# Kernel tuning notes

Measured on AMD Instinct MI355X. Metric: run time of the kernel, lower is better.

## Reference

```python
import jax, jax.numpy as jnp
import numpy as np

N_NODES = 50000
N_EDGES = 300000
D = 256
EPS = 1e-12


def setup_inputs() -> dict:
    key = jax.random.key(0)
    ks = jax.random.split(key, 10)
    h5_all = jax.random.normal(ks[0], (N_NODES, D), dtype=jnp.float32)
    edge_index = jax.random.randint(ks[1], (2, N_EDGES), 0, N_NODES, dtype=jnp.int64)
    edge_weight = jax.random.uniform(ks[2], (N_EDGES,), dtype=jnp.float32)
    s = 1.0 / np.sqrt(D)
    W6 = jax.random.normal(ks[3], (D, D), dtype=jnp.float32) * s
    b6 = jnp.zeros((D,), dtype=jnp.float32)
    W7 = jax.random.normal(ks[4], (D, D), dtype=jnp.float32) * s
    b7 = jnp.zeros((D,), dtype=jnp.float32)
    Wp = jax.random.normal(ks[5], (D, D), dtype=jnp.float32) * s
    bp = jnp.zeros((D,), dtype=jnp.float32)
    return {"h5_all": h5_all, "edge_index": edge_index, "edge_weight": edge_weight,
            "W6": W6, "b6": b6, "W7": W7, "b7": b7, "Wp": Wp, "bp": bp}


def _gcn_layer(x, W, b, src, dst, norm, n_nodes):
    # x: [N, D]; transform then gather-scale-scatter along edges
    xt = x @ W                                   # [N, D]
    msg = xt[src] * norm[:, None]                # [E, D] gathered + scaled
    agg = jax.ops.segment_sum(msg, dst, num_segments=n_nodes)  # [N, D]
    return jax.nn.relu(agg + b)


def reference(h5_all, edge_index, edge_weight, W6, b6, W7, b7, Wp, bp):
    src, dst = edge_index[0], edge_index[1]
    # symmetric degree normalization with edge weights (GCN-style)
    deg_out = jax.ops.segment_sum(edge_weight, src, num_segments=N_NODES)
    deg_in = jax.ops.segment_sum(edge_weight, dst, num_segments=N_NODES)
    norm = edge_weight * jax.lax.rsqrt(deg_out[src] * deg_in[dst] + EPS)  # [E]
    h6 = _gcn_layer(h5_all, W6, b6, src, dst, norm, N_NODES)
    h7 = _gcn_layer(h6, W7, b7, src, dst, norm, N_NODES)
    out = h7 @ Wp + bp                           # post_mp linear head
    return out
```

## Files before the change

kernel.cpp:

```cpp
#include <hip/hip_runtime.h>

#define N_NODES 50000
#define N_PANELS 3125
#define N_EDGES 300000
#define EPS_F 1e-12f
#define DEGB 64
#define WB 96
#define AB (N_NODES * 32 / 256)
#define FILLB 128
#define GB 512
#define SCAN_NB ((N_NODES + 255) / 256)
#define ZBYTES (N_NODES * 8)

typedef _Float16 f16x8 __attribute__((ext_vector_type(8)));
typedef float f32x4 __attribute__((ext_vector_type(4)));

static __device__ inline f32x4 mfma_f16(f16x8 a, f16x8 b, f32x4 c) {
    return __builtin_amdgcn_mfma_f32_16x16x32_f16(a, b, c, 0, 0, 0);
}

static __device__ inline size_t swz(int row, int l) {
    return ((size_t)(row >> 4) * 8 + (l >> 2)) * 512 + (size_t)((l & 3) * 128 + (row & 15) * 8);
}


__global__ __launch_bounds__(256) void zero_kernel(int4* __restrict__ p, int n16) {
    int i = blockIdx.x * 256 + threadIdx.x;
    if (i < n16) p[i] = make_int4(0, 0, 0, 0);
}


__global__ __launch_bounds__(256) void p1_kernel(const int* __restrict__ ei,
                                                 const float* __restrict__ ew,
                                                 unsigned* __restrict__ pk_out,
                                                 unsigned* __restrict__ pk_in,
                                                 unsigned* __restrict__ rank,
                                                 const float* __restrict__ W6,
                                                 const float* __restrict__ W7,
                                                 const float* __restrict__ Wp,
                                                 _Float16* __restrict__ Bsw,
                                                 const float* __restrict__ h5,
                                                 _Float16* __restrict__ Asw) {
    int b = blockIdx.x;
    if (b < DEGB) {
        for (int e = b * 256 + (int)threadIdx.x; e < N_EDGES; e += DEGB * 256) {
            int s = ei[e];
            int d = ei[N_EDGES + e];
            unsigned wfx = (unsigned)(ew[e] * 262144.0f);
            atomicAdd(&pk_out[s], wfx);
            unsigned old = atomicAdd(&pk_in[d], (1u << 24) | wfx);
            rank[e] = old >> 24;
        }
    } else if (b < DEGB + WB) {
        int bb = b - DEGB;
        int wsel = bb >> 5;
        const float* W = (wsel == 0) ? W6 : (wsel == 1) ? W7 : Wp;
        int id = (bb & 31) * 256 + threadIdx.x;
        int n = id >> 5, l = id & 31;
        f16x8 o;
#pragma unroll
        for (int j = 0; j < 8; ++j)
            o[j] = (_Float16)W[(l * 8 + j) * 256 + n];
        *(f16x8*)&Bsw[(size_t)wsel * 65536 + swz(n, l)] = o;
    } else {
        int tid = (b - DEGB - WB) * 256 + threadIdx.x;
        int row = tid >> 5, l = tid & 31;
        const float* p = &h5[(size_t)row * 256 + l * 8];
        float4 v0 = *(const float4*)p;
        float4 v1 = *(const float4*)(p + 4);
        f16x8 o;
        o[0] = (_Float16)v0.x; o[1] = (_Float16)v0.y;
        o[2] = (_Float16)v0.z; o[3] = (_Float16)v0.w;
        o[4] = (_Float16)v1.x; o[5] = (_Float16)v1.y;
        o[6] = (_Float16)v1.z; o[7] = (_Float16)v1.w;
        *(f16x8*)&Asw[swz(row, l)] = o;
    }
}


__global__ __launch_bounds__(256) void scan1_kernel(const unsigned* __restrict__ pk_in,
                                                    const unsigned* __restrict__ pk_out,
                                                    float* __restrict__ deg_in,
                                                    float* __restrict__ deg_out,
                                                    int* __restrict__ partial) {
    __shared__ int sh[256];
    int i = blockIdx.x * 256 + threadIdx.x;
    int c = 0;
    if (i < N_NODES) {
        unsigned p = pk_in[i];
        c = (int)(p >> 24);
        deg_in[i] = (float)(p & 0xFFFFFFu) * 0x1p-18f;
        deg_out[i] = (float)pk_out[i] * 0x1p-18f;
    }
    sh[threadIdx.x] = c;
    __syncthreads();
    for (int off = 128; off > 0; off >>= 1) {
        if (threadIdx.x < (unsigned)off) sh[threadIdx.x] += sh[threadIdx.x + off];
        __syncthreads();
    }
    if (threadIdx.x == 0) partial[blockIdx.x] = sh[0];
}

__global__ __launch_bounds__(256) void scan23_kernel(const unsigned* __restrict__ pk_in,
                                                     const int* __restrict__ partial,
                                                     int* __restrict__ row_ptr) {
    __shared__ int ps[256];
    __shared__ int sh[256];
    int t = threadIdx.x;
    int pv = (t < SCAN_NB) ? partial[t] : 0;
    ps[t] = pv;
    __syncthreads();
    for (int off = 1; off < 256; off <<= 1) {
        int x = (t >= off) ? ps[t - off] : 0;
        __syncthreads();
        ps[t] += x;
        __syncthreads();
    }
    int incl = ps[t];
    __syncthreads();
    ps[t] = incl - pv;
    __syncthreads();
    const int boff = ps[blockIdx.x];

    int i = blockIdx.x * 256 + t;
    int v = (i < N_NODES) ? (int)(pk_in[i] >> 24) : 0;
    sh[t] = v;
    __syncthreads();
    for (int off = 1; off < 256; off <<= 1) {
        int x = (t >= off) ? sh[t - off] : 0;
        __syncthreads();
        sh[t] += x;
        __syncthreads();
    }
    if (i < N_NODES) row_ptr[i] = sh[t] - v + boff;
    if (i == 0) row_ptr[N_NODES] = N_EDGES;
}


__global__ __launch_bounds__(256) void p2_kernel(const int* __restrict__ ei,
                                                 const float* __restrict__ ew,
                                                 const unsigned* __restrict__ rank,
                                                 const float* __restrict__ deg_out,
                                                 const float* __restrict__ deg_in,
                                                 const int* __restrict__ row_ptr,
                                                 int2* __restrict__ csr,
                                                 const _Float16* __restrict__ Asw,
                                                 const _Float16* __restrict__ Bsw,
                                                 _Float16* __restrict__ xt) {
    __shared__ __align__(16) _Float16 ebuf[4][16 * 72];

    if (blockIdx.x < FILLB) {
        for (int e = blockIdx.x * 256 + (int)threadIdx.x; e < N_EDGES; e += FILLB * 256) {
            int s = ei[e];
            int d = ei[N_EDGES + e];
            float nm = ew[e] * rsqrtf(deg_out[s] * deg_in[d] + EPS_F);
            csr[row_ptr[d] + (int)rank[e]] = make_int2(s, __float_as_int(nm));
        }
        return;
    }

    const int t = threadIdx.x;
    const int w = t >> 6, lane = t & 63;

    f16x8 bf[4][8];
#pragma unroll
    for (int cp4 = 0; cp4 < 4; ++cp4)
#pragma unroll
        for (int kb = 0; kb < 8; ++kb)
            bf[cp4][kb] = *(const f16x8*)&Bsw[(size_t)((w * 4 + cp4) * 8 + kb) * 512 + lane * 8];

    for (int p = blockIdx.x - FILLB; p < N_PANELS; p += GB) {
        const _Float16* abase = &Asw[(size_t)p * 4096 + lane * 8];
        f16x8 af[8];
#pragma unroll
        for (int kb = 0; kb < 8; ++kb)
            af[kb] = *(const f16x8*)&abase[kb * 512];

        f32x4 acc[4];
#pragma unroll
        for (int cp4 = 0; cp4 < 4; ++cp4) acc[cp4] = (f32x4){0.f, 0.f, 0.f, 0.f};
#pragma unroll
        for (int kb = 0; kb < 8; ++kb)
#pragma unroll
            for (int cp4 = 0; cp4 < 4; ++cp4)
                acc[cp4] = mfma_f16(af[kb], bf[cp4][kb], acc[cp4]);

        _Float16* eb = ebuf[w];
        const int rq = 4 * (lane >> 4);
        const int lr = lane & 15;
#pragma unroll
        for (int cp4 = 0; cp4 < 4; ++cp4)
#pragma unroll
            for (int rr = 0; rr < 4; ++rr)
                eb[(rq + rr) * 72 + cp4 * 16 + lr] = (_Float16)acc[cp4][rr];
#pragma unroll
        for (int it = 0; it < 2; ++it) {
            int rl = it * 8 + (lane >> 3);
            f16x8 v = *(const f16x8*)&eb[rl * 72 + (lane & 7) * 8];
            *(f16x8*)&xt[(size_t)(p * 16 + rl) * 256 + w * 64 + (lane & 7) * 8] = v;
        }
    }
}


template <int MODE>
__global__ __launch_bounds__(256) void gemm_f16(const _Float16* __restrict__ Asw,
                                                const _Float16* __restrict__ Bsw,
                                                const float* __restrict__ bias,
                                                void* __restrict__ Cout) {
    __shared__ __align__(16) char ebraw[4][16 * 68 * 4];

    const int t = threadIdx.x;
    const int w = t >> 6, lane = t & 63;
    const int lr = lane & 15;

    f16x8 bf[4][8];
#pragma unroll
    for (int cp4 = 0; cp4 < 4; ++cp4)
#pragma unroll
        for (int kb = 0; kb < 8; ++kb)
            bf[cp4][kb] = *(const f16x8*)&Bsw[(size_t)((w * 4 + cp4) * 8 + kb) * 512 + lane * 8];

    float bc[4];
    if (MODE == 1) {
#pragma unroll
        for (int cp4 = 0; cp4 < 4; ++cp4) bc[cp4] = bias[w * 64 + cp4 * 16 + lr];
    }

    for (int p = blockIdx.x; p < N_PANELS; p += GB) {
        const _Float16* abase = &Asw[(size_t)p * 4096 + lane * 8];
        f16x8 af[8];
#pragma unroll
        for (int kb = 0; kb < 8; ++kb)
            af[kb] = *(const f16x8*)&abase[kb * 512];

        f32x4 acc[4];
#pragma unroll
        for (int cp4 = 0; cp4 < 4; ++cp4) acc[cp4] = (f32x4){0.f, 0.f, 0.f, 0.f};
#pragma unroll
        for (int kb = 0; kb < 8; ++kb)
#pragma unroll
            for (int cp4 = 0; cp4 < 4; ++cp4)
                acc[cp4] = mfma_f16(af[kb], bf[cp4][kb], acc[cp4]);

        const int rq = 4 * (lane >> 4);
        if (MODE == 0) {
            _Float16* eb = (_Float16*)ebraw[w];
#pragma unroll
            for (int cp4 = 0; cp4 < 4; ++cp4)
#pragma unroll
                for (int rr = 0; rr < 4; ++rr)
                    eb[(rq + rr) * 72 + cp4 * 16 + lr] = (_Float16)acc[cp4][rr];
            _Float16* xp = (_Float16*)Cout;
#pragma unroll
            for (int it = 0; it < 2; ++it) {
                int rl = it * 8 + (lane >> 3);
                f16x8 v = *(const f16x8*)&eb[rl * 72 + (lane & 7) * 8];
                *(f16x8*)&xp[(size_t)(p * 16 + rl) * 256 + w * 64 + (lane & 7) * 8] = v;
            }
        } else {
            float* eb = (float*)ebraw[w];
#pragma unroll
            for (int cp4 = 0; cp4 < 4; ++cp4)
#pragma unroll
                for (int rr = 0; rr < 4; ++rr)
                    eb[(rq + rr) * 68 + cp4 * 16 + lr] = acc[cp4][rr] + bc[cp4];
            float* op = (float*)Cout;
#pragma unroll
            for (int it = 0; it < 4; ++it) {
                int rl = it * 4 + (lane >> 4);
                float4 v = *(const float4*)&eb[rl * 68 + lr * 4];
                *(float4*)&op[(size_t)(p * 16 + rl) * 256 + w * 64 + lr * 4] = v;
            }
        }
    }
}


__global__ __launch_bounds__(256) void agg_kernel(const _Float16* __restrict__ xt,
                                                  const int* __restrict__ row_ptr,
                                                  const int2* __restrict__ csr,
                                                  const float* __restrict__ bias,
                                                  _Float16* __restrict__ Asw) {
    const int g = threadIdx.x >> 5;
    const int l = threadIdx.x & 31;
    const int v = blockIdx.x * 8 + g;
    const int d0 = l * 8;

    const int s0 = row_ptr[v];
    const int s1 = row_ptr[v + 1];

    float acc[8] = {0.f, 0.f, 0.f, 0.f, 0.f, 0.f, 0.f, 0.f};

    int i = s0;
    for (; i + 4 <= s1; i += 4) {
        int2 hd[4];
#pragma unroll
        for (int u = 0; u < 4; ++u) hd[u] = csr[i + u];
        f16x8 val[4];
#pragma unroll
        for (int u = 0; u < 4; ++u)
            val[u] = *(const f16x8*)&xt[(size_t)hd[u].x * 256 + d0];
#pragma unroll
        for (int u = 0; u < 4; ++u) {
            float wv = __int_as_float(hd[u].y);
#pragma unroll
            for (int j = 0; j < 8; ++j)
                acc[j] += (float)val[u][j] * wv;
        }
    }
    {
        int rem = s1 - i;
        int2 hd[3];
#pragma unroll
        for (int u = 0; u < 3; ++u)
            hd[u] = (u < rem) ? csr[i + u] : make_int2(0, 0);
        f16x8 val[3];
#pragma unroll
        for (int u = 0; u < 3; ++u)
            val[u] = *(const f16x8*)&xt[(size_t)hd[u].x * 256 + d0];
#pragma unroll
        for (int u = 0; u < 3; ++u) {
            float wv = __int_as_float(hd[u].y);
#pragma unroll
            for (int j = 0; j < 8; ++j)
                acc[j] += (float)val[u][j] * wv;
        }
    }

    f16x8 o;
#pragma unroll
    for (int j = 0; j < 8; ++j) {
        float r = acc[j] + bias[d0 + j];
        r = r > 0.f ? r : 0.f;
        o[j] = (_Float16)r;
    }
    *(f16x8*)&Asw[swz(v, l)] = o;
}


extern "C" void kernel_launch(void* const* d_in, const int* in_sizes, int n_in,
                              void* d_out, int out_size, void* d_ws, size_t ws_size,
                              hipStream_t stream) {
    (void)in_sizes; (void)n_in; (void)out_size; (void)ws_size;
    const float* h5 = (const float*)d_in[0];
    const int*   ei = (const int*)d_in[1];
    const float* ew = (const float*)d_in[2];
    const float* W6 = (const float*)d_in[3];
    const float* b6 = (const float*)d_in[4];
    const float* W7 = (const float*)d_in[5];
    const float* b7 = (const float*)d_in[6];
    const float* Wp = (const float*)d_in[7];
    const float* bp = (const float*)d_in[8];
    float* out = (float*)d_out;

    char* ws = (char*)d_ws;
    size_t off = 0;
    auto alloc = [&](size_t bytes) -> void* {
        void* p = ws + off;
        off = (off + bytes + 255) & ~(size_t)255;
        return p;
    };

    char* zblk = (char*)alloc(ZBYTES);
    unsigned* pk_out = (unsigned*)zblk;
    unsigned* pk_in  = (unsigned*)(zblk + N_NODES * 4);

    unsigned* rank  = (unsigned*)alloc(N_EDGES * 4);
    float* deg_out = (float*)alloc(N_NODES * 4);
    float* deg_in  = (float*)alloc(N_NODES * 4);
    int*   row_ptr = (int*)alloc((N_NODES + 1) * 4);
    int*   partial = (int*)alloc(SCAN_NB * 4);
    int2*  csr     = (int2*)alloc(N_EDGES * 8);
    _Float16* Bsw  = (_Float16*)alloc(3 * 65536 * 2);
    _Float16* Asw  = (_Float16*)alloc((size_t)N_NODES * 256 * 2);
    _Float16* xt   = (_Float16*)alloc((size_t)N_NODES * 256 * 2);

    const int Z16 = ZBYTES / 16;

    zero_kernel<<<(Z16 + 255) / 256, 256, 0, stream>>>((int4*)zblk, Z16);

    p1_kernel<<<DEGB + WB + AB, 256, 0, stream>>>(ei, ew, pk_out, pk_in, rank,
                                                  W6, W7, Wp, Bsw, h5, Asw);

    scan1_kernel<<<SCAN_NB, 256, 0, stream>>>(pk_in, pk_out, deg_in, deg_out, partial);
    scan23_kernel<<<SCAN_NB, 256, 0, stream>>>(pk_in, partial, row_ptr);

    p2_kernel<<<FILLB + GB, 256, 0, stream>>>(ei, ew, rank, deg_out, deg_in, row_ptr,
                                              csr, Asw, Bsw, xt);

    agg_kernel<<<N_NODES / 8, 256, 0, stream>>>(xt, row_ptr, csr, b6, Asw);
    gemm_f16<0><<<GB, 256, 0, stream>>>(Asw, Bsw + 65536, nullptr, xt);
    agg_kernel<<<N_NODES / 8, 256, 0, stream>>>(xt, row_ptr, csr, b7, Asw);
    gemm_f16<1><<<GB, 256, 0, stream>>>(Asw, Bsw + 2 * 65536, bp, out);
}
```

Measured before the change: 160.5 us.

## Fuse h5 fp16 conversion into first GEMM and reschedule setup kernels

The first transform GEMM now reads h5 in fp32 directly, converts it to fp16 through a shared-memory tile, and multiplies, so the separate swizzled Asw staging pass, with its write and reread of a 25 MB fp16 copy, is gone. The zeroing and weight swizzle are merged into one init kernel. The degree atomics now run alongside the GEMM, and the CSR fill moves to its own kernel after the scan. This adds two block barriers per panel and makes the CSR fill a standalone launch that no longer overlaps the GEMM.

```diff
diff --git a/kernel.cpp b/kernel.cpp
--- a/kernel.cpp
+++ b/kernel.cpp
@@ -5,8 +5,8 @@
 #define N_EDGES 300000
 #define EPS_F 1e-12f
 #define DEGB 64
+#define ZB 98
 #define WB 96
-#define AB (N_NODES * 32 / 256)
 #define FILLB 128
 #define GB 512
 #define SCAN_NB ((N_NODES + 255) / 256)
@@ -24,23 +24,41 @@
 }
 
 
-__global__ __launch_bounds__(256) void zero_kernel(int4* __restrict__ p, int n16) {
-    int i = blockIdx.x * 256 + threadIdx.x;
-    if (i < n16) p[i] = make_int4(0, 0, 0, 0);
-}
-
-
-__global__ __launch_bounds__(256) void p1_kernel(const int* __restrict__ ei,
+__global__ __launch_bounds__(256) void init_kernel(int4* __restrict__ z,
+                                                   const float* __restrict__ W6,
+                                                   const float* __restrict__ W7,
+                                                   const float* __restrict__ Wp,
+                                                   _Float16* __restrict__ Bsw) {
+    int b = blockIdx.x;
+    if (b < ZB) {
+        int i = b * 256 + threadIdx.x;
+        if (i < ZBYTES / 16) z[i] = make_int4(0, 0, 0, 0);
+    } else {
+        int bb = b - ZB;
+        int wsel = bb >> 5;
+        const float* W = (wsel == 0) ? W6 : (wsel == 1) ? W7 : Wp;
+        int id = (bb & 31) * 256 + threadIdx.x;
+        int n = id >> 5, l = id & 31;
+        f16x8 o;
+#pragma unroll
+        for (int j = 0; j < 8; ++j)
+            o[j] = (_Float16)W[(l * 8 + j) * 256 + n];
+        *(f16x8*)&Bsw[(size_t)wsel * 65536 + swz(n, l)] = o;
+    }
+}
+
+
+__global__ __launch_bounds__(256) void pA_kernel(const int* __restrict__ ei,
                                                  const float* __restrict__ ew,
                                                  unsigned* __restrict__ pk_out,
                                                  unsigned* __restrict__ pk_in,
                                                  unsigned* __restrict__ rank,
-                                                 const float* __restrict__ W6,
-                                                 const float* __restrict__ W7,
-                                                 const float* __restrict__ Wp,
-                                                 _Float16* __restrict__ Bsw,
                                                  const float* __restrict__ h5,
-                                                 _Float16* __restrict__ Asw) {
+                                                 const _Float16* __restrict__ Bsw,
+                                                 _Float16* __restrict__ xt) {
+    __shared__ __align__(16) _Float16 atile[16 * 264];
+    __shared__ __align__(16) _Float16 ebuf[4][16 * 72];
+
     int b = blockIdx.x;
     if (b < DEGB) {
         for (int e = b * 256 + (int)threadIdx.x; e < N_EDGES; e += DEGB * 256) {
@@ -51,29 +69,67 @@
             unsigned old = atomicAdd(&pk_in[d], (1u << 24) | wfx);
             rank[e] = old >> 24;
         }
-    } else if (b < DEGB + WB) {
-        int bb = b - DEGB;
-        int wsel = bb >> 5;
-        const float* W = (wsel == 0) ? W6 : (wsel == 1) ? W7 : Wp;
-        int id = (bb & 31) * 256 + threadIdx.x;
-        int n = id >> 5, l = id & 31;
-        f16x8 o;
-#pragma unroll
-        for (int j = 0; j < 8; ++j)
-            o[j] = (_Float16)W[(l * 8 + j) * 256 + n];
-        *(f16x8*)&Bsw[(size_t)wsel * 65536 + swz(n, l)] = o;
-    } else {
-        int tid = (b - DEGB - WB) * 256 + threadIdx.x;
-        int row = tid >> 5, l = tid & 31;
-        const float* p = &h5[(size_t)row * 256 + l * 8];
-        float4 v0 = *(const float4*)p;
-        float4 v1 = *(const float4*)(p + 4);
-        f16x8 o;
-        o[0] = (_Float16)v0.x; o[1] = (_Float16)v0.y;
-        o[2] = (_Float16)v0.z; o[3] = (_Float16)v0.w;
-        o[4] = (_Float16)v1.x; o[5] = (_Float16)v1.y;
-        o[6] = (_Float16)v1.z; o[7] = (_Float16)v1.w;
-        *(f16x8*)&Asw[swz(row, l)] = o;
+        return;
+    }
+
+    const int t = threadIdx.x;
+    const int w = t >> 6, lane = t & 63;
+    const int srow = t >> 4;
+    const int scol = (t & 15) * 16;
+
+    f16x8 bf[4][8];
+#pragma unroll
+    for (int cp4 = 0; cp4 < 4; ++cp4)
+#pragma unroll
+        for (int kb = 0; kb < 8; ++kb)
+            bf[cp4][kb] = *(const f16x8*)&Bsw[(size_t)((w * 4 + cp4) * 8 + kb) * 512 + lane * 8];
+
+    for (int p = b - DEGB; p < N_PANELS; p += GB) {
+        const float* src = &h5[(size_t)(p * 16 + srow) * 256 + scol];
+        f16x8 c0, c1;
+#pragma unroll
+        for (int q = 0; q < 2; ++q) {
+            float4 v0 = *(const float4*)(src + q * 8);
+            float4 v1 = *(const float4*)(src + q * 8 + 4);
+            f16x8& cc = q ? c1 : c0;
+            cc[0] = (_Float16)v0.x; cc[1] = (_Float16)v0.y;
+            cc[2] = (_Float16)v0.z; cc[3] = (_Float16)v0.w;
+            cc[4] = (_Float16)v1.x; cc[5] = (_Float16)v1.y;
+            cc[6] = (_Float16)v1.z; cc[7] = (_Float16)v1.w;
+        }
+        *(f16x8*)&atile[srow * 264 + scol] = c0;
+        *(f16x8*)&atile[srow * 264 + scol + 8] = c1;
+        __syncthreads();
+
+        f16x8 af[8];
+#pragma unroll
+        for (int kb = 0; kb < 8; ++kb)
+            af[kb] = *(const f16x8*)&atile[(lane & 15) * 264 + kb * 32 + (lane >> 4) * 8];
+        __syncthreads();
+
+        f32x4 acc[4];
+#pragma unroll
+        for (int cp4 = 0; cp4 < 4; ++cp4) acc[cp4] = (f32x4){0.f, 0.f, 0.f, 0.f};
+#pragma unroll
+        for (int kb = 0; kb < 8; ++kb)
+#pragma unroll
+            for (int cp4 = 0; cp4 < 4; ++cp4)
+                acc[cp4] = mfma_f16(af[kb], bf[cp4][kb], acc[cp4]);
+
+        _Float16* eb = ebuf[w];
+        const int rq = 4 * (lane >> 4);
+        const int lr = lane & 15;
+#pragma unroll
+        for (int cp4 = 0; cp4 < 4; ++cp4)
+#pragma unroll
+            for (int rr = 0; rr < 4; ++rr)
+                eb[(rq + rr) * 72 + cp4 * 16 + lr] = (_Float16)acc[cp4][rr];
+#pragma unroll
+        for (int it = 0; it < 2; ++it) {
+            int rl = it * 8 + (lane >> 3);
+            f16x8 v = *(const f16x8*)&eb[rl * 72 + (lane & 7) * 8];
+            *(f16x8*)&xt[(size_t)(p * 16 + rl) * 256 + w * 64 + (lane & 7) * 8] = v;
+        }
     }
 }
 
@@ -137,68 +193,18 @@
 }
 
 
-__global__ __launch_bounds__(256) void p2_kernel(const int* __restrict__ ei,
-                                                 const float* __restrict__ ew,
-                                                 const unsigned* __restrict__ rank,
-                                                 const float* __restrict__ deg_out,
-                                                 const float* __restrict__ deg_in,
-                                                 const int* __restrict__ row_ptr,
-                                                 int2* __restrict__ csr,
-                                                 const _Float16* __restrict__ Asw,
-                                                 const _Float16* __restrict__ Bsw,
-                                                 _Float16* __restrict__ xt) {
-    __shared__ __align__(16) _Float16 ebuf[4][16 * 72];
-
-    if (blockIdx.x < FILLB) {
-        for (int e = blockIdx.x * 256 + (int)threadIdx.x; e < N_EDGES; e += FILLB * 256) {
-            int s = ei[e];
-            int d = ei[N_EDGES + e];
-            float nm = ew[e] * rsqrtf(deg_out[s] * deg_in[d] + EPS_F);
-            csr[row_ptr[d] + (int)rank[e]] = make_int2(s, __float_as_int(nm));
-        }
-        return;
-    }
-
-    const int t = threadIdx.x;
-    const int w = t >> 6, lane = t & 63;
-
-    f16x8 bf[4][8];
-#pragma unroll
-    for (int cp4 = 0; cp4 < 4; ++cp4)
-#pragma unroll
-        for (int kb = 0; kb < 8; ++kb)
-            bf[cp4][kb] = *(const f16x8*)&Bsw[(size_t)((w * 4 + cp4) * 8 + kb) * 512 + lane * 8];
-
-    for (int p = blockIdx.x - FILLB; p < N_PANELS; p += GB) {
-        const _Float16* abase = &Asw[(size_t)p * 4096 + lane * 8];
-        f16x8 af[8];
-#pragma unroll
-        for (int kb = 0; kb < 8; ++kb)
-            af[kb] = *(const f16x8*)&abase[kb * 512];
-
-        f32x4 acc[4];
-#pragma unroll
-        for (int cp4 = 0; cp4 < 4; ++cp4) acc[cp4] = (f32x4){0.f, 0.f, 0.f, 0.f};
-#pragma unroll
-        for (int kb = 0; kb < 8; ++kb)
-#pragma unroll
-            for (int cp4 = 0; cp4 < 4; ++cp4)
-                acc[cp4] = mfma_f16(af[kb], bf[cp4][kb], acc[cp4]);
-
-        _Float16* eb = ebuf[w];
-        const int rq = 4 * (lane >> 4);
-        const int lr = lane & 15;
-#pragma unroll
-        for (int cp4 = 0; cp4 < 4; ++cp4)
-#pragma unroll
-            for (int rr = 0; rr < 4; ++rr)
-                eb[(rq + rr) * 72 + cp4 * 16 + lr] = (_Float16)acc[cp4][rr];
-#pragma unroll
-        for (int it = 0; it < 2; ++it) {
-            int rl = it * 8 + (lane >> 3);
-            f16x8 v = *(const f16x8*)&eb[rl * 72 + (lane & 7) * 8];
-            *(f16x8*)&xt[(size_t)(p * 16 + rl) * 256 + w * 64 + (lane & 7) * 8] = v;
-        }
+__global__ __launch_bounds__(256) void fill_kernel(const int* __restrict__ ei,
+                                                   const float* __restrict__ ew,
+                                                   const unsigned* __restrict__ rank,
+                                                   const float* __restrict__ deg_out,
+                                                   const float* __restrict__ deg_in,
+                                                   const int* __restrict__ row_ptr,
+                                                   int2* __restrict__ csr) {
+    for (int e = blockIdx.x * 256 + (int)threadIdx.x; e < N_EDGES; e += FILLB * 256) {
+        int s = ei[e];
+        int d = ei[N_EDGES + e];
+        float nm = ew[e] * rsqrtf(deg_out[s] * deg_in[d] + EPS_F);
+        csr[row_ptr[d] + (int)rank[e]] = make_int2(s, __float_as_int(nm));
     }
 }
 
@@ -376,18 +382,14 @@
     _Float16* Asw  = (_Float16*)alloc((size_t)N_NODES * 256 * 2);
     _Float16* xt   = (_Float16*)alloc((size_t)N_NODES * 256 * 2);
 
-    const int Z16 = ZBYTES / 16;
-
-    zero_kernel<<<(Z16 + 255) / 256, 256, 0, stream>>>((int4*)zblk, Z16);
-
-    p1_kernel<<<DEGB + WB + AB, 256, 0, stream>>>(ei, ew, pk_out, pk_in, rank,
-                                                  W6, W7, Wp, Bsw, h5, Asw);
+    init_kernel<<<ZB + WB, 256, 0, stream>>>((int4*)zblk, W6, W7, Wp, Bsw);
+
+    pA_kernel<<<DEGB + GB, 256, 0, stream>>>(ei, ew, pk_out, pk_in, rank, h5, Bsw, xt);
 
     scan1_kernel<<<SCAN_NB, 256, 0, stream>>>(pk_in, pk_out, deg_in, deg_out, partial);
     scan23_kernel<<<SCAN_NB, 256, 0, stream>>>(pk_in, partial, row_ptr);
 
-    p2_kernel<<<FILLB + GB, 256, 0, stream>>>(ei, ew, rank, deg_out, deg_in, row_ptr,
-                                              csr, Asw, Bsw, xt);
+    fill_kernel<<<FILLB, 256, 0, stream>>>(ei, ew, rank, deg_out, deg_in, row_ptr, csr);
 
     agg_kernel<<<N_NODES / 8, 256, 0, stream>>>(xt, row_ptr, csr, b6, Asw);
     gemm_f16<0><<<GB, 256, 0, stream>>>(Asw, Bsw + 65536, nullptr, xt);
```

Measured after the change: 146.1 us. 1.1x faster.
